# Kernel tuning notes

Measured on AMD Instinct MI355X. Metric: run time of the kernel, lower is better.

Reference implementation:

```python
import jax, jax.numpy as jnp
import numpy as np
import itertools

B = 128
K = 3            # number of element types == len(n_list)
C_IN = 256
C_OUT = 256
N_LIST = [3, 3, 3]  # L = 9, P = 9!/(3!3!3!) = 1680


def _build_mask():
    # multiset [0,0,0,1,1,1,2,2,2]; distinct permutations of it
    base = []
    for i, n in enumerate(N_LIST):
        base += [i] * n
    perms = sorted(set(itertools.permutations(base)))  # deterministic order
    idx = np.array(perms, dtype=np.int32)              # (P, L)
    # M[a, p, l] = 1.0 iff idx[p, l] == a  -> (K, P, L) binary mask
    M = np.stack([(idx == a).astype(np.float32) for a in range(K)], 0)
    return jnp.asarray(M), idx.shape[1]


def setup_inputs() -> dict:
    key = jax.random.key(0)
    kx, kw = jax.random.split(key)
    M, L = _build_mask()
    x = jax.random.normal(kx, (B, L, C_IN), dtype=jnp.float32)
    # weightParameter: (k, channels_out, channels_in)
    W = jax.random.normal(kw, (K, C_OUT, C_IN), dtype=jnp.float32)
    return {"x": x, "W": W, "M": M}


def reference(x, W, M):
    # Original: for each type a, W_a = x @ W[a].T (B,L,Cout), then
    # y += einsum('BNC,PN->BPC', W_a, M[a]).  Fused over the k loop:
    # Z[b,l,a,o] = sum_c x[b,l,c] * W[a,o,c]   (small: B*L*K*Cout)
    Z = jnp.einsum('blc,koc->blko', x, W)
    # y[b,p,o] = sum_{a,l} Z[b,l,a,o] * M[a,p,l]
    y = jnp.einsum('blko,kpl->bpo', Z, M)
    return y
```

## Files before the change

kernel.cpp:

```cpp
#include <hip/hip_runtime.h>

#define B_DIM 128
#define L_DIM 9
#define K_DIM 3
#define C 256
#define P_TOT 1680
#define R_DIM 27
#define TILE_P 80
#define TILES 21

#define WS_Z_OFF 131072

typedef float vfloat4 __attribute__((ext_vector_type(4)));

__device__ inline float4 add4(float4 a, float4 b) {
    return make_float4(a.x + b.x, a.y + b.y, a.z + b.z, a.w + b.w);
}

__global__ void prep_kernel(const float* __restrict__ M,
                            uint2* __restrict__ packed) {
    int p = blockIdx.x * blockDim.x + threadIdx.x;
    if (p >= P_TOT) return;
    unsigned rows[L_DIM];
#pragma unroll
    for (int l = 0; l < L_DIM; ++l) {
        float m1 = M[(1 * P_TOT + p) * L_DIM + l];
        float m2 = M[(2 * P_TOT + p) * L_DIM + l];
        unsigned a = (unsigned)(m1 + 2.0f * m2 + 0.5f);
        rows[l] = (unsigned)(l * K_DIM) + a;
    }
    unsigned d = 0;
    if (p > 0) {
        while (d < L_DIM) {
            float m1 = M[(1 * P_TOT + (p - 1)) * L_DIM + d];
            float m2 = M[(2 * P_TOT + (p - 1)) * L_DIM + d];
            unsigned pr = d * K_DIM + (unsigned)(m1 + 2.0f * m2 + 0.5f);
            if (pr != rows[d]) break;
            ++d;
        }
    }
    unsigned lo = 0, hi = 0;
#pragma unroll
    for (int l = 0; l < 6; ++l) lo |= rows[l] << (5 * l);
#pragma unroll
    for (int l = 6; l < L_DIM; ++l) hi |= rows[l] << (5 * (l - 6));
    hi |= d << 15;
    packed[p] = make_uint2(lo, hi);
}

__global__ __launch_bounds__(256) void z_kernel(const float* __restrict__ x,
                                                const float* __restrict__ W,
                                                float* __restrict__ Z) {
    __shared__ float red[L_DIM * 128];

    int bid = blockIdx.x;
    int b = bid / 6;
    int rem = bid % 6;
    int a = rem >> 1;
    int ohalf = rem & 1;
    int t = threadIdx.x & 127;
    int chalf = threadIdx.x >> 7;
    int o = ohalf * 128 + t;

    const float4* __restrict__ W4 =
        (const float4*)(W + (size_t)(a * C + o) * C) + chalf * 32;
    const float4* __restrict__ X4 =
        (const float4*)(x + (size_t)b * L_DIM * C) + chalf * 32;

    float acc[L_DIM];
#pragma unroll
    for (int l = 0; l < L_DIM; ++l) acc[l] = 0.0f;

#pragma unroll 8
    for (int c4 = 0; c4 < C / 8; ++c4) {
        float4 wv = W4[c4];
#pragma unroll
        for (int l = 0; l < L_DIM; ++l) {
            float4 xv = X4[l * (C / 4) + c4];
            acc[l] += wv.x * xv.x + wv.y * xv.y + wv.z * xv.z + wv.w * xv.w;
        }
    }
    if (chalf) {
#pragma unroll
        for (int l = 0; l < L_DIM; ++l) red[l * 128 + t] = acc[l];
    }
    __syncthreads();
    if (!chalf) {
        float* zb = Z + (size_t)b * R_DIM * C;
#pragma unroll
        for (int l = 0; l < L_DIM; ++l)
            zb[(l * K_DIM + a) * C + o] = acc[l] + red[l * 128 + t];
    }
}

__global__ __launch_bounds__(256) void y_kernel(const float* __restrict__ Z,
                                                const uint2* __restrict__ packed,
                                                float* __restrict__ out) {
    __shared__ float Zs[R_DIM * C];
    __shared__ uint2 pk[TILE_P];

    int bid = blockIdx.x;
    int b = bid / TILES;
    int tile = bid % TILES;
    int base = tile * TILE_P;

    const float4* Zb4 = (const float4*)(Z + (size_t)b * R_DIM * C);
    float4* Zs4 = (float4*)Zs;
    for (int i = threadIdx.x; i < R_DIM * (C / 4); i += 256) Zs4[i] = Zb4[i];
    if (threadIdx.x < TILE_P) pk[threadIdx.x] = packed[base + threadIdx.x];
    __syncthreads();

    int wave = threadIdx.x >> 6;
    int lane = threadIdx.x & 63;
    const float4* zsr = (const float4*)Zs;
    vfloat4* out4 = (vfloat4*)out;

    float4 p0, p1, p2, p3, p4, p5, p6, p7, p8;

    int pl = wave * (TILE_P / 4);
    for (int j = 0; j < TILE_P / 4; ++j, ++pl) {
        uint2 w = pk[pl];
        unsigned lo = __builtin_amdgcn_readfirstlane(w.x);
        unsigned hi = __builtin_amdgcn_readfirstlane(w.y);
        int k = (j == 0) ? 0 : (int)(hi >> 15);
        switch (k) {
            case 0: p0 = zsr[(lo & 31u) * 64 + lane]; [[fallthrough]];
            case 1: p1 = add4(p0, zsr[((lo >> 5) & 31u) * 64 + lane]); [[fallthrough]];
            case 2: p2 = add4(p1, zsr[((lo >> 10) & 31u) * 64 + lane]); [[fallthrough]];
            case 3: p3 = add4(p2, zsr[((lo >> 15) & 31u) * 64 + lane]); [[fallthrough]];
            case 4: p4 = add4(p3, zsr[((lo >> 20) & 31u) * 64 + lane]); [[fallthrough]];
            case 5: p5 = add4(p4, zsr[((lo >> 25) & 31u) * 64 + lane]); [[fallthrough]];
            case 6: p6 = add4(p5, zsr[(hi & 31u) * 64 + lane]); [[fallthrough]];
            case 7: p7 = add4(p6, zsr[((hi >> 5) & 31u) * 64 + lane]); [[fallthrough]];
            case 8: p8 = add4(p7, zsr[((hi >> 10) & 31u) * 64 + lane]); break;
            default: break;
        }
        int orow = b * P_TOT + base + pl;
        vfloat4 sv = {p8.x, p8.y, p8.z, p8.w};
        __builtin_nontemporal_store(sv, &out4[(size_t)orow * 64 + lane]);
    }
}

extern "C" void kernel_launch(void* const* d_in, const int* in_sizes, int n_in,
                              void* d_out, int out_size, void* d_ws, size_t ws_size,
                              hipStream_t stream) {
    const float* x = (const float*)d_in[0];
    const float* W = (const float*)d_in[1];
    const float* M = (const float*)d_in[2];
    float* out = (float*)d_out;

    uint2* packed = (uint2*)d_ws;
    float* Z = (float*)((char*)d_ws + WS_Z_OFF);

    prep_kernel<<<(P_TOT + 255) / 256, 256, 0, stream>>>(M, packed);
    z_kernel<<<B_DIM * K_DIM * 2, 256, 0, stream>>>(x, W, Z);
    y_kernel<<<B_DIM * TILES, 256, 0, stream>>>(Z, packed, out);
}
```

Measured before the change: 273.8 us.

## Fuse Z projection into output kernel and pre-transpose W in setup

Merges the Z computation and the permutation-sum kernel into one 1024-thread block per (batch, half of P), computing Z straight into shared memory so it no longer round-trips through global memory. W is transposed once in a combined setup kernel so each thread reads weights coalesced by output channel. The launch drops from 3 kernels to 2. In exchange each block recomputes the full Z for its batch (done twice per batch), the grid shrinks to only 256 large blocks, and a quarter of threads sit idle during the matmul phase.

```diff
diff --git a/kernel.cpp b/kernel.cpp
--- a/kernel.cpp
+++ b/kernel.cpp
@@ -6,10 +6,9 @@
 #define C 256
 #define P_TOT 1680
 #define R_DIM 27
-#define TILE_P 80
-#define TILES 21
+#define HALF_P 840
 
-#define WS_Z_OFF 131072
+#define WS_WT_OFF 16384
 
 typedef float vfloat4 __attribute__((ext_vector_type(4)));
 
@@ -17,112 +16,108 @@
     return make_float4(a.x + b.x, a.y + b.y, a.z + b.z, a.w + b.w);
 }
 
-__global__ void prep_kernel(const float* __restrict__ M,
-                            uint2* __restrict__ packed) {
-    int p = blockIdx.x * blockDim.x + threadIdx.x;
-    if (p >= P_TOT) return;
-    unsigned rows[L_DIM];
-#pragma unroll
-    for (int l = 0; l < L_DIM; ++l) {
-        float m1 = M[(1 * P_TOT + p) * L_DIM + l];
-        float m2 = M[(2 * P_TOT + p) * L_DIM + l];
-        unsigned a = (unsigned)(m1 + 2.0f * m2 + 0.5f);
-        rows[l] = (unsigned)(l * K_DIM) + a;
-    }
-    unsigned d = 0;
-    if (p > 0) {
-        while (d < L_DIM) {
-            float m1 = M[(1 * P_TOT + (p - 1)) * L_DIM + d];
-            float m2 = M[(2 * P_TOT + (p - 1)) * L_DIM + d];
-            unsigned pr = d * K_DIM + (unsigned)(m1 + 2.0f * m2 + 0.5f);
-            if (pr != rows[d]) break;
-            ++d;
-        }
-    }
-    unsigned lo = 0, hi = 0;
-#pragma unroll
-    for (int l = 0; l < 6; ++l) lo |= rows[l] << (5 * l);
-#pragma unroll
-    for (int l = 6; l < L_DIM; ++l) hi |= rows[l] << (5 * (l - 6));
-    hi |= d << 15;
-    packed[p] = make_uint2(lo, hi);
-}
-
-__global__ __launch_bounds__(256) void z_kernel(const float* __restrict__ x,
-                                                const float* __restrict__ W,
-                                                float* __restrict__ Z) {
-    __shared__ float red[L_DIM * 128];
-
+__global__ __launch_bounds__(256) void setup_kernel(const float* __restrict__ M,
+                                                    const float* __restrict__ W,
+                                                    uint2* __restrict__ packed,
+                                                    float* __restrict__ Wt) {
     int bid = blockIdx.x;
-    int b = bid / 6;
-    int rem = bid % 6;
-    int a = rem >> 1;
-    int ohalf = rem & 1;
-    int t = threadIdx.x & 127;
-    int chalf = threadIdx.x >> 7;
-    int o = ohalf * 128 + t;
-
-    const float4* __restrict__ W4 =
-        (const float4*)(W + (size_t)(a * C + o) * C) + chalf * 32;
-    const float4* __restrict__ X4 =
-        (const float4*)(x + (size_t)b * L_DIM * C) + chalf * 32;
-
-    float acc[L_DIM];
-#pragma unroll
-    for (int l = 0; l < L_DIM; ++l) acc[l] = 0.0f;
-
-#pragma unroll 8
-    for (int c4 = 0; c4 < C / 8; ++c4) {
-        float4 wv = W4[c4];
+    int t = threadIdx.x;
+    if (bid < 7) {
+        int p = bid * 256 + t;
+        if (p >= P_TOT) return;
+        unsigned rows[L_DIM];
 #pragma unroll
         for (int l = 0; l < L_DIM; ++l) {
-            float4 xv = X4[l * (C / 4) + c4];
-            acc[l] += wv.x * xv.x + wv.y * xv.y + wv.z * xv.z + wv.w * xv.w;
+            float m1 = M[(1 * P_TOT + p) * L_DIM + l];
+            float m2 = M[(2 * P_TOT + p) * L_DIM + l];
+            unsigned a = (unsigned)(m1 + 2.0f * m2 + 0.5f);
+            rows[l] = (unsigned)(l * K_DIM) + a;
         }
-    }
-    if (chalf) {
+        unsigned d = 0;
+        if (p > 0) {
+            while (d < L_DIM) {
+                float m1 = M[(1 * P_TOT + (p - 1)) * L_DIM + d];
+                float m2 = M[(2 * P_TOT + (p - 1)) * L_DIM + d];
+                unsigned pr = d * K_DIM + (unsigned)(m1 + 2.0f * m2 + 0.5f);
+                if (pr != rows[d]) break;
+                ++d;
+            }
+        }
+        unsigned lo = 0, hi = 0;
 #pragma unroll
-        for (int l = 0; l < L_DIM; ++l) red[l * 128 + t] = acc[l];
-    }
-    __syncthreads();
-    if (!chalf) {
-        float* zb = Z + (size_t)b * R_DIM * C;
+        for (int l = 0; l < 6; ++l) lo |= rows[l] << (5 * l);
 #pragma unroll
-        for (int l = 0; l < L_DIM; ++l)
-            zb[(l * K_DIM + a) * C + o] = acc[l] + red[l * 128 + t];
+        for (int l = 6; l < L_DIM; ++l) hi |= rows[l] << (5 * (l - 6));
+        hi |= d << 15;
+        packed[p] = make_uint2(lo, hi);
+    } else {
+        int tb = bid - 7;
+#pragma unroll
+        for (int i = 0; i < 4; ++i) {
+            int rowid = tb * 4 + i;
+            int a = rowid >> 8;
+            int c = rowid & 255;
+            Wt[(a * C + c) * C + t] = W[(a * C + t) * C + c];
+        }
     }
 }
 
-__global__ __launch_bounds__(256) void y_kernel(const float* __restrict__ Z,
-                                                const uint2* __restrict__ packed,
-                                                float* __restrict__ out) {
+__global__ __launch_bounds__(1024) void fused_kernel(const float* __restrict__ x,
+                                                     const uint2* __restrict__ packed,
+                                                     const float* __restrict__ Wt,
+                                                     float* __restrict__ out) {
+    __shared__ float xs[L_DIM * C];
     __shared__ float Zs[R_DIM * C];
-    __shared__ uint2 pk[TILE_P];
+    __shared__ uint2 pk[HALF_P];
 
     int bid = blockIdx.x;
-    int b = bid / TILES;
-    int tile = bid % TILES;
-    int base = tile * TILE_P;
+    int b = bid >> 1;
+    int pstart = (bid & 1) * HALF_P;
+    int t = threadIdx.x;
 
-    const float4* Zb4 = (const float4*)(Z + (size_t)b * R_DIM * C);
-    float4* Zs4 = (float4*)Zs;
-    for (int i = threadIdx.x; i < R_DIM * (C / 4); i += 256) Zs4[i] = Zb4[i];
-    if (threadIdx.x < TILE_P) pk[threadIdx.x] = packed[base + threadIdx.x];
+    if (t < L_DIM * C / 4) ((float4*)xs)[t] = ((const float4*)(x + (size_t)b * L_DIM * C))[t];
+    if (t < HALF_P) pk[t] = packed[pstart + t];
     __syncthreads();
 
-    int wave = threadIdx.x >> 6;
-    int lane = threadIdx.x & 63;
+    int o = t & 255;
+    int slot = t >> 8;
+    if (slot < K_DIM) {
+        const float* __restrict__ wp = Wt + (size_t)slot * C * C + o;
+        float acc[L_DIM];
+#pragma unroll
+        for (int l = 0; l < L_DIM; ++l) acc[l] = 0.0f;
+#pragma unroll 2
+        for (int c4 = 0; c4 < C / 4; ++c4) {
+            float w0 = wp[(4 * c4 + 0) * C];
+            float w1 = wp[(4 * c4 + 1) * C];
+            float w2 = wp[(4 * c4 + 2) * C];
+            float w3 = wp[(4 * c4 + 3) * C];
+#pragma unroll
+            for (int l = 0; l < L_DIM; ++l) {
+                float4 xv = ((const float4*)xs)[l * (C / 4) + c4];
+                acc[l] += xv.x * w0 + xv.y * w1 + xv.z * w2 + xv.w * w3;
+            }
+        }
+#pragma unroll
+        for (int l = 0; l < L_DIM; ++l) Zs[(l * K_DIM + slot) * C + o] = acc[l];
+    }
+    __syncthreads();
+
+    int wave = t >> 6;
+    int lane = t & 63;
     const float4* zsr = (const float4*)Zs;
     vfloat4* out4 = (vfloat4*)out;
 
+    int pb = (HALF_P * wave) >> 4;
+    int pe = (HALF_P * (wave + 1)) >> 4;
+
     float4 p0, p1, p2, p3, p4, p5, p6, p7, p8;
 
-    int pl = wave * (TILE_P / 4);
-    for (int j = 0; j < TILE_P / 4; ++j, ++pl) {
+    for (int pl = pb; pl < pe; ++pl) {
         uint2 w = pk[pl];
         unsigned lo = __builtin_amdgcn_readfirstlane(w.x);
         unsigned hi = __builtin_amdgcn_readfirstlane(w.y);
-        int k = (j == 0) ? 0 : (int)(hi >> 15);
+        int k = (pl == pb) ? 0 : (int)(hi >> 15);
         switch (k) {
             case 0: p0 = zsr[(lo & 31u) * 64 + lane]; [[fallthrough]];
             case 1: p1 = add4(p0, zsr[((lo >> 5) & 31u) * 64 + lane]); [[fallthrough]];
@@ -135,9 +130,9 @@
             case 8: p8 = add4(p7, zsr[((hi >> 10) & 31u) * 64 + lane]); break;
             default: break;
         }
-        int orow = b * P_TOT + base + pl;
+        size_t orow = (size_t)(b * P_TOT + pstart + pl);
         vfloat4 sv = {p8.x, p8.y, p8.z, p8.w};
-        __builtin_nontemporal_store(sv, &out4[(size_t)orow * 64 + lane]);
+        __builtin_nontemporal_store(sv, &out4[orow * 64 + lane]);
     }
 }
 
@@ -150,9 +145,8 @@
     float* out = (float*)d_out;
 
     uint2* packed = (uint2*)d_ws;
-    float* Z = (float*)((char*)d_ws + WS_Z_OFF);
+    float* Wt = (float*)((char*)d_ws + WS_WT_OFF);
 
-    prep_kernel<<<(P_TOT + 255) / 256, 256, 0, stream>>>(M, packed);
-    z_kernel<<<B_DIM * K_DIM * 2, 256, 0, stream>>>(x, W, Z);
-    y_kernel<<<B_DIM * TILES, 256, 0, stream>>>(Z, packed, out);
+    setup_kernel<<<199, 256, 0, stream>>>(M, W, packed, Wt);
+    fused_kernel<<<B_DIM * 2, 1024, 0, stream>>>(x, packed, Wt, out);
 }
```

After: 262.3 us. 4.2% less time.
